# Performance work log

Hardware: AMD Instinct MI355X
Metric: run time of the kernel (lower is better)

Reference implementation:

```python
import jax, jax.numpy as jnp
import numpy as np

B, NMASK, DIM, HEADS = 8, 1024, 768, 12
HEAD_DIM = DIM // HEADS
SCALE = HEAD_DIM ** -0.5
NEG = -1e9  # finite stand-in for -inf to keep fully-masked rows NaN-free


def setup_inputs() -> dict:
    key = jax.random.key(0)
    ks = jax.random.split(key, 7)
    x = jax.random.normal(ks[0], (B, NMASK + 1, DIM), dtype=jnp.float32)
    # valid-prefix padding mask (realistic variable-length batch), lengths >= 1
    lengths = jax.random.randint(ks[1], (B,), 1, NMASK + 1)
    mask = jnp.arange(NMASK)[None, :] < lengths[:, None]  # (B, NMASK) bool
    w_qkv = jax.random.normal(ks[2], (DIM, 3 * DIM), dtype=jnp.float32) * (DIM ** -0.5)
    b_qkv = jax.random.normal(ks[3], (3 * DIM,), dtype=jnp.float32) * 0.02
    w_proj = jax.random.normal(ks[4], (DIM, DIM), dtype=jnp.float32) * (DIM ** -0.5)
    b_proj = jax.random.normal(ks[5], (DIM,), dtype=jnp.float32) * 0.02
    return {"x": x, "mask": mask, "w_qkv": w_qkv, "b_qkv": b_qkv,
            "w_proj": w_proj, "b_proj": b_proj}


def reference(x, mask, w_qkv, b_qkv, w_proj, b_proj):
    b, n, _ = x.shape
    qkv = x @ w_qkv + b_qkv                        # (b, n, 3*dim)
    qkv = qkv.reshape(b, n, 3, HEADS, HEAD_DIM)    # 'b n (qkv h d)'
    qkv = jnp.transpose(qkv, (2, 0, 3, 1, 4))      # (3, b, h, n, d)
    q, k, v = qkv[0], qkv[1], qkv[2]
    logits = jnp.einsum('bhid,bhjd->bhij', q, k) * SCALE
    m = jnp.pad(mask, ((0, 0), (1, 0)), constant_values=True)   # prepend CLS=True
    am = m[:, None, :] & m[:, :, None]             # (b, n, n)
    logits = jnp.where(am[:, None, :, :], logits, NEG)
    attn = jax.nn.softmax(logits, axis=-1)
    out = jnp.einsum('bhij,bhjd->bhid', attn, v)   # (b, h, n, d)
    out = jnp.transpose(out, (0, 2, 1, 3)).reshape(b, n, DIM)
    return out @ w_proj + b_proj                   # dropout is identity (eval/p=0)
```

## Files before the change

### kernel.cpp

```cpp
#include <hip/hip_runtime.h>
#include <stdint.h>

#define BATCH   8
#define NMASK_  1024
#define SEQ     1025
#define NPAD    1056
#define DIM     768
#define HEADS   12
#define HD      64
#define BHN     (BATCH*HEADS)
#define MROWS   (BATCH*SEQ)
#define K3      (3*DIM)

typedef unsigned short u16;
typedef __attribute__((ext_vector_type(8))) short s8v;
typedef __attribute__((ext_vector_type(4))) float f4v;
typedef __attribute__((ext_vector_type(4))) unsigned short u16x4;

__device__ __forceinline__ u16 rne_bf16(float f) {
  unsigned u = __float_as_uint(f);
  u += 0x7fffu + ((u >> 16) & 1u);
  return (u16)(u >> 16);
}
__device__ __forceinline__ float bf2f(u16 u) {
  return __uint_as_float(((unsigned)u) << 16);
}

__device__ __forceinline__ void gld16(const u16* g, u16* l) {
  __builtin_amdgcn_global_load_lds(
      (const __attribute__((address_space(1))) void*)g,
      (__attribute__((address_space(3))) void*)l, 16, 0, 0);
}

__global__ __launch_bounds__(256) void k_len(const int* __restrict__ mask,
                                             int* __restrict__ lens) {
  int b = blockIdx.x, t = threadIdx.x;
  int s = 0;
  for (int j = t; j < NMASK_; j += 256) s += (mask[b * NMASK_ + j] != 0) ? 1 : 0;
  __shared__ int red[256];
  red[t] = s; __syncthreads();
  for (int st = 128; st > 0; st >>= 1) { if (t < st) red[t] += red[t + st]; __syncthreads(); }
  if (t == 0) lens[b] = red[0] + 1;
}

__global__ __launch_bounds__(256) void k_cvt_x(const float* __restrict__ x,
                                               u16* __restrict__ xb, int n4) {
  int i = blockIdx.x * 256 + threadIdx.x;
  if (i >= n4) return;
  float4 v = ((const float4*)x)[i];
  u16x4 o;
  o[0] = rne_bf16(v.x); o[1] = rne_bf16(v.y); o[2] = rne_bf16(v.z); o[3] = rne_bf16(v.w);
  *(u16x4*)&xb[i * 4] = o;
}

__global__ __launch_bounds__(256) void k_wT(const float* __restrict__ w,
                                            u16* __restrict__ wT, int R, int C) {
  __shared__ float tile[32][33];
  int c0 = blockIdx.x * 32, r0 = blockIdx.y * 32;
  int tx = threadIdx.x & 31, ty = threadIdx.x >> 5;
  #pragma unroll
  for (int i = 0; i < 32; i += 8) tile[ty + i][tx] = w[(size_t)(r0 + ty + i) * C + c0 + tx];
  __syncthreads();
  #pragma unroll
  for (int i = 0; i < 32; i += 8)
    wT[(size_t)(c0 + ty + i) * R + r0 + tx] = rne_bf16(tile[tx][ty + i]);
}

__global__ __launch_bounds__(256) void k_zpad(u16* __restrict__ VT) {
  int idx = blockIdx.x * 256 + threadIdx.x;
  const int PADW = NPAD - SEQ;
  if (idx >= BHN * HD * PADW) return;
  int c = idx % PADW, rd = idx / PADW;
  VT[(size_t)rd * NPAD + SEQ + c] = 0;
}

__device__ __forceinline__ void gemm_ml128(const u16* __restrict__ A,
                                           const u16* __restrict__ Bt,
                                           int M, int m0, int n0,
                                           f4v acc[4][4], u16* smem) {
  u16* lA = smem;
  u16* lB = smem + 4096;
  const int t = threadIdx.x;
  const int w = t >> 6, l = t & 63, lg = l >> 4, lr = l & 15;
  const int wr = w >> 1, wc = w & 1;

  int rA0 = m0 + (t >> 2);       if (rA0 >= M) rA0 = M - 1;
  int rA1 = m0 + (t >> 2) + 64;  if (rA1 >= M) rA1 = M - 1;
  const u16* sA0 = A  + (size_t)rA0 * DIM + (t & 3) * 8;
  const u16* sA1 = A  + (size_t)rA1 * DIM + (t & 3) * 8;
  const u16* sB0 = Bt + (size_t)(n0 + (t >> 2)) * DIM + (t & 3) * 8;
  const u16* sB1 = Bt + (size_t)(n0 + (t >> 2) + 64) * DIM + (t & 3) * 8;
  u16* dA0 = &lA[w * 512];
  u16* dA1 = &lA[2048 + w * 512];
  u16* dB0 = &lB[w * 512];
  u16* dB1 = &lB[2048 + w * 512];

  #pragma unroll
  for (int fm = 0; fm < 4; fm++)
    #pragma unroll
    for (int fn = 0; fn < 4; fn++) { f4v z = {0.f, 0.f, 0.f, 0.f}; acc[fm][fn] = z; }

  for (int k0 = 0; k0 < DIM; k0 += 32) {
    __syncthreads();
    gld16(sA0, dA0); gld16(sA1, dA1);
    gld16(sB0, dB0); gld16(sB1, dB1);
    sA0 += 32; sA1 += 32; sB0 += 32; sB1 += 32;
    __syncthreads();
    s8v a[4], bb[4];
    #pragma unroll
    for (int fm = 0; fm < 4; fm++) a[fm] = *(const s8v*)&lA[(wr * 64 + fm * 16 + lr) * 32 + lg * 8];
    #pragma unroll
    for (int fn = 0; fn < 4; fn++) bb[fn] = *(const s8v*)&lB[(wc * 64 + fn * 16 + lr) * 32 + lg * 8];
    #pragma unroll
    for (int fm = 0; fm < 4; fm++)
      #pragma unroll
      for (int fn = 0; fn < 4; fn++)
        acc[fm][fn] = __builtin_amdgcn_mfma_f32_16x16x32_bf16(a[fm], bb[fn], acc[fm][fn], 0, 0, 0);
  }
}

__global__ __launch_bounds__(256) void k_gemm_qkv(const u16* __restrict__ xb,
                                                  const u16* __restrict__ wqkvT,
                                                  const float* __restrict__ bqkv,
                                                  const int* __restrict__ lens,
                                                  u16* __restrict__ Q,
                                                  u16* __restrict__ Kb,
                                                  u16* __restrict__ VT) {
  __shared__ alignas(16) u16 smem[16384];
  int m0 = blockIdx.x * 128, n0 = blockIdx.y * 128;
  const int which = n0 / DIM;
  if (which < 2) {
    int b0 = m0 / SEQ, off = m0 - b0 * SEQ;
    bool spans = (m0 + 127) >= (b0 + 1) * SEQ;
    if (!spans && off >= lens[b0]) return;
  }
  f4v acc[4][4];
  gemm_ml128(xb, wqkvT, MROWS, m0, n0, acc, smem);
  const int t = threadIdx.x;
  const int w = t >> 6, l = t & 63, lg = l >> 4, lr = l & 15;
  const int wr = w >> 1, wc = w & 1;
  const int hbase = (n0 - which * DIM) >> 6;
  const float qs = (which == 0) ? 0.125f : 1.0f;

  __syncthreads();
  #pragma unroll
  for (int fn = 0; fn < 4; fn++) {
    int col = wc * 64 + fn * 16 + lr;
    float bias = bqkv[n0 + col];
    #pragma unroll
    for (int fm = 0; fm < 4; fm++)
      #pragma unroll
      for (int r = 0; r < 4; r++) {
        int row = wr * 64 + fm * 16 + lg * 4 + r;
        smem[row * 128 + col] = rne_bf16((acc[fm][fn][r] + bias) * qs);
      }
  }
  __syncthreads();

  if (which < 2) {
    u16* dst = (which == 0) ? Q : Kb;
    #pragma unroll
    for (int p = 0; p < 8; p++) {
      int c = p * 256 + t;
      int row = c >> 4, col = (c & 15) * 8;
      int gm = m0 + row;
      if (gm >= MROWS) continue;
      int b = gm / SEQ, n = gm - b * SEQ;
      int head = hbase + (col >> 6), d = col & 63;
      *(s8v*)&dst[((size_t)(b * HEADS + head) * NPAD + n) * HD + d] =
          *(const s8v*)&smem[row * 128 + col];
    }
  } else {
    #pragma unroll
    for (int p = 0; p < 8; p++) {
      int c = p * 256 + t;
      int d = c & 127, nb = c >> 7;
      int gm0 = m0 + nb * 8;
      if (gm0 >= MROWS) continue;
      int head = hbase + (d >> 6), dl = d & 63;
      int b0 = gm0 / SEQ;
      if (gm0 + 7 < MROWS && (gm0 + 7) < (b0 + 1) * SEQ) {
        s8v v;
        #pragma unroll
        for (int e = 0; e < 8; e++) v[e] = (short)smem[(nb * 8 + e) * 128 + d];
        int n = gm0 - b0 * SEQ;
        *(s8v*)&VT[((size_t)(b0 * HEADS + head) * HD + dl) * NPAD + n] = v;
      } else {
        for (int e = 0; e < 8; e++) {
          int gm = gm0 + e;
          if (gm >= MROWS) break;
          int b = gm / SEQ, n = gm - b * SEQ;
          VT[((size_t)(b * HEADS + head) * HD + dl) * NPAD + n] = smem[(nb * 8 + e) * 128 + d];
        }
      }
    }
  }
}

__global__ __launch_bounds__(256) void k_vmean(const u16* __restrict__ VT,
                                               float* __restrict__ vmean) {
  int bh = blockIdx.x, t = threadIdx.x;
  int d = t >> 2, part = t & 3;
  const u16* row = VT + (size_t)(bh * HD + d) * NPAD;
  float s = 0.f;
  for (int jc = part * 264; jc < part * 264 + 264; jc += 8) {
    if (jc + 8 <= SEQ) {
      s8v v = *(const s8v*)&row[jc];
      #pragma unroll
      for (int e = 0; e < 8; e++) s += bf2f((u16)v[e]);
    } else {
      for (int e = 0; e < 8; e++) if (jc + e < SEQ) s += bf2f(row[jc + e]);
    }
  }
  __shared__ float red[256];
  red[t] = s; __syncthreads();
  if (part == 0)
    vmean[bh * HD + d] = (red[t] + red[t + 1] + red[t + 2] + red[t + 3]) * (1.0f / (float)SEQ);
}

__global__ __launch_bounds__(256) void k_vproj(const float* __restrict__ vmean,
                                               const u16* __restrict__ wprojT,
                                               const float* __restrict__ bproj,
                                               float* __restrict__ vproj) {
  int gid = blockIdx.x * 4 + (threadIdx.x >> 6);
  if (gid >= BATCH * DIM) return;
  int b = gid / DIM, n = gid - b * DIM;
  int l = threadIdx.x & 63;
  const u16* wr = wprojT + (size_t)n * DIM;
  const float* vm = vmean + b * DIM;
  float s = 0.f;
  #pragma unroll
  for (int i = 0; i < DIM / 64; ++i)
    s += vm[l + i * 64] * bf2f(wr[l + i * 64]);
  #pragma unroll
  for (int off = 32; off >= 1; off >>= 1) s += __shfl_xor(s, off);
  if (l == 0) vproj[gid] = s + bproj[n];
}

__global__ __launch_bounds__(256) void k_attn(const u16* __restrict__ Q,
                                              const u16* __restrict__ Kb,
                                              const u16* __restrict__ VT,
                                              const int* __restrict__ lens,
                                              u16* __restrict__ aout) {
  int bh = blockIdx.x; int b = bh / HEADS, h = bh - b * HEADS;
  int Lp1 = lens[b];
  int q0 = blockIdx.y * 64;
  if (q0 >= Lp1) return;
  __shared__ alignas(16) u16 Kt[64 * 64];
  __shared__ alignas(16) u16 Vt[64 * 64];
  __shared__ alignas(16) u16 Pt[4][16 * 72];
  const int t = threadIdx.x, w = t >> 6, l = t & 63, lg = l >> 4, lr = l & 15;
  const u16* Qbh = Q  + (size_t)bh * NPAD * HD;
  const u16* Kbh = Kb + (size_t)bh * NPAD * HD;
  const u16* Vbh = VT + (size_t)bh * HD * NPAD;

  int qi = q0 + w * 16 + lr;
  s8v qf[2];
  qf[0] = *(const s8v*)&Qbh[(size_t)qi * HD +      lg * 8];
  qf[1] = *(const s8v*)&Qbh[(size_t)qi * HD + 32 + lg * 8];

  f4v o[4];
  #pragma unroll
  for (int fd = 0; fd < 4; fd++) { f4v z = {0.f, 0.f, 0.f, 0.f}; o[fd] = z; }
  float mrow[4], ssacc[4];
  #pragma unroll
  for (int r = 0; r < 4; r++) { mrow[r] = -1e30f; ssacc[r] = 0.f; }

  const int js = t >> 2, cs = t & 3;
  const u16* kSrc = Kbh + (size_t)js * HD   + cs * 8;
  const u16* vSrc = Vbh + (size_t)js * NPAD + cs * 8;
  const int kDst0 = js * 64 + ((cs       ^ (js & 7)) * 8);
  const int kDst1 = js * 64 + (((cs + 4) ^ (js & 7)) * 8);
  s8v kr0, kr1, vr0, vr1;
  kr0 = *(const s8v*)(kSrc);        kr1 = *(const s8v*)(kSrc + 32);
  vr0 = *(const s8v*)(vSrc);        vr1 = *(const s8v*)(vSrc + 32);

  for (int j0 = 0; j0 < Lp1; j0 += 64) {
    __syncthreads();
    *(s8v*)&Kt[kDst0] = kr0;  *(s8v*)&Kt[kDst1] = kr1;
    *(s8v*)&Vt[kDst0] = vr0;  *(s8v*)&Vt[kDst1] = vr1;
    if (j0 + 64 < Lp1) {
      kr0 = *(const s8v*)(kSrc + (size_t)(j0 + 64) * HD);
      kr1 = *(const s8v*)(kSrc + (size_t)(j0 + 64) * HD + 32);
      vr0 = *(const s8v*)(vSrc + (j0 + 64));
      vr1 = *(const s8v*)(vSrc + (j0 + 64) + 32);
    }
    __syncthreads();

    f4v sf[4];
    #pragma unroll
    for (int jf = 0; jf < 4; jf++) { f4v z = {0.f,0.f,0.f,0.f}; sf[jf] = z; }
    __builtin_amdgcn_s_setprio(1);
    #pragma unroll
    for (int jf = 0; jf < 4; jf++) {
      int j = jf * 16 + lr;
      #pragma unroll
      for (int kf = 0; kf < 2; kf++) {
        s8v kfr = *(const s8v*)&Kt[j * 64 + (((kf * 4 + lg) ^ (j & 7)) * 8)];
        sf[jf] = __builtin_amdgcn_mfma_f32_16x16x32_bf16(qf[kf], kfr, sf[jf], 0, 0, 0);
      }
    }
    __builtin_amdgcn_s_setprio(0);

    float sv[4][4], pmax[4];
    if (j0 + 64 <= Lp1) {
      #pragma unroll
      for (int r = 0; r < 4; r++) {
        sv[r][0] = sf[0][r]; sv[r][1] = sf[1][r];
        sv[r][2] = sf[2][r]; sv[r][3] = sf[3][r];
        float tm = fmaxf(fmaxf(sv[r][0], sv[r][1]), fmaxf(sv[r][2], sv[r][3]));
        tm = fmaxf(tm, __shfl_xor(tm, 1)); tm = fmaxf(tm, __shfl_xor(tm, 2));
        tm = fmaxf(tm, __shfl_xor(tm, 4)); tm = fmaxf(tm, __shfl_xor(tm, 8));
        pmax[r] = tm;
      }
    } else {
      bool ok[4];
      #pragma unroll
      for (int jf = 0; jf < 4; jf++) ok[jf] = (j0 + jf * 16 + lr) < Lp1;
      #pragma unroll
      for (int r = 0; r < 4; r++) {
        sv[r][0] = ok[0] ? sf[0][r] : -1e30f;
        sv[r][1] = ok[1] ? sf[1][r] : -1e30f;
        sv[r][2] = ok[2] ? sf[2][r] : -1e30f;
        sv[r][3] = ok[3] ? sf[3][r] : -1e30f;
        float tm = fmaxf(fmaxf(sv[r][0], sv[r][1]), fmaxf(sv[r][2], sv[r][3]));
        tm = fmaxf(tm, __shfl_xor(tm, 1)); tm = fmaxf(tm, __shfl_xor(tm, 2));
        tm = fmaxf(tm, __shfl_xor(tm, 4)); tm = fmaxf(tm, __shfl_xor(tm, 8));
        pmax[r] = tm;
      }
    }
    bool ng = (pmax[0] <= mrow[0] + 8.f) && (pmax[1] <= mrow[1] + 8.f) &&
              (pmax[2] <= mrow[2] + 8.f) && (pmax[3] <= mrow[3] + 8.f);
    if (!__all(ng)) {
      #pragma unroll
      for (int r = 0; r < 4; r++) {
        float nm = fmaxf(mrow[r], pmax[r]);
        float fs = __expf(mrow[r] - nm);
        mrow[r] = nm;
        ssacc[r] *= fs;
        o[0][r] *= fs; o[1][r] *= fs; o[2][r] *= fs; o[3][r] *= fs;
      }
    }
    u16* P = &Pt[w][0];
    #pragma unroll
    for (int r = 0; r < 4; r++) {
      float e0 = __expf(sv[r][0] - mrow[r]);
      float e1 = __expf(sv[r][1] - mrow[r]);
      float e2 = __expf(sv[r][2] - mrow[r]);
      float e3 = __expf(sv[r][3] - mrow[r]);
      int prow = (lg * 4 + r) * 72;
      P[prow +      lr] = rne_bf16(e0);
      P[prow + 16 + lr] = rne_bf16(e1);
      P[prow + 32 + lr] = rne_bf16(e2);
      P[prow + 48 + lr] = rne_bf16(e3);
      ssacc[r] += (e0 + e1) + (e2 + e3);
    }
    asm volatile("s_waitcnt lgkmcnt(0)" ::: "memory");
    s8v pa[2];
    pa[0] = *(const s8v*)&P[lr * 72 +      lg * 8];
    pa[1] = *(const s8v*)&P[lr * 72 + 32 + lg * 8];
    __builtin_amdgcn_s_setprio(1);
    #pragma unroll
    for (int fd = 0; fd < 4; fd++) {
      int dv = fd * 16 + lr;
      #pragma unroll
      for (int kf = 0; kf < 2; kf++) {
        s8v vb = *(const s8v*)&Vt[dv * 64 + (((kf * 4 + lg) ^ (dv & 7)) * 8)];
        o[fd] = __builtin_amdgcn_mfma_f32_16x16x32_bf16(pa[kf], vb, o[fd], 0, 0, 0);
      }
    }
    __builtin_amdgcn_s_setprio(0);
  }

  float inv[4];
  #pragma unroll
  for (int r = 0; r < 4; r++) {
    float rs = ssacc[r];
    rs += __shfl_xor(rs, 1); rs += __shfl_xor(rs, 2);
    rs += __shfl_xor(rs, 4); rs += __shfl_xor(rs, 8);
    inv[r] = 1.0f / rs;
  }
  #pragma unroll
  for (int fd = 0; fd < 4; fd++)
    #pragma unroll
    for (int r = 0; r < 4; r++) {
      int i = q0 + w * 16 + lg * 4 + r;
      if (i < Lp1)
        aout[(size_t)(b * SEQ + i) * DIM + h * HD + fd * 16 + lr] = rne_bf16(o[fd][r] * inv[r]);
    }
}

__global__ __launch_bounds__(256) void k_bcast(const int* __restrict__ lens,
                                               const float* __restrict__ vproj,
                                               float* __restrict__ out) {
  int idx = blockIdx.x * 256 + threadIdx.x;
  if (idx >= MROWS * DIM / 4) return;
  int e4 = idx * 4;
  int b = e4 / (SEQ * DIM);
  int rem = e4 - b * (SEQ * DIM);
  int i = rem / DIM;
  if (i >= lens[b]) {
    int c = rem - i * DIM;
    const float* vp = &vproj[b * DIM + c];
    float4 v = { vp[0], vp[1], vp[2], vp[3] };
    ((float4*)out)[idx] = v;
  }
}

__global__ __launch_bounds__(256) void k_gemm_proj(const u16* __restrict__ aout,
                                                   const u16* __restrict__ wprojT,
                                                   const float* __restrict__ bproj,
                                                   const int* __restrict__ lens,
                                                   float* __restrict__ out) {
  __shared__ alignas(16) u16 smem[16384];
  int m0 = blockIdx.x * 128, n0 = blockIdx.y * 128;
  {
    int b0 = m0 / SEQ, off = m0 - b0 * SEQ;
    bool spans = (m0 + 127) >= (b0 + 1) * SEQ;
    if (!spans && off >= lens[b0]) return;
  }
  f4v acc[4][4];
  gemm_ml128(aout, wprojT, MROWS, m0, n0, acc, smem);
  const int t = threadIdx.x;
  const int w = t >> 6, l = t & 63, lg = l >> 4, lr = l & 15;
  const int wr = w >> 1, wc = w & 1;
  #pragma unroll
  for (int fn = 0; fn < 4; fn++) {
    int gc = n0 + wc * 64 + fn * 16 + lr;
    float bias = bproj[gc];
    #pragma unroll
    for (int fm = 0; fm < 4; fm++)
      #pragma unroll
      for (int r = 0; r < 4; r++) {
        int gm = m0 + wr * 64 + fm * 16 + lg * 4 + r;
        if (gm < MROWS) out[(size_t)gm * DIM + gc] = acc[fm][fn][r] + bias;
      }
  }
}

extern "C" void kernel_launch(void* const* d_in, const int* in_sizes, int n_in,
                              void* d_out, int out_size, void* d_ws, size_t ws_size,
                              hipStream_t stream) {
  const float* x      = (const float*)d_in[0];
  const int*   mask   = (const int*)  d_in[1];
  const float* w_qkv  = (const float*)d_in[2];
  const float* b_qkv  = (const float*)d_in[3];
  const float* w_proj = (const float*)d_in[4];
  const float* b_proj = (const float*)d_in[5];
  float* out = (float*)d_out;

  u16* xb     = (u16*)d_ws;
  u16* wqkvT  = xb    + (size_t)MROWS * DIM;
  u16* wprojT = wqkvT + (size_t)K3 * DIM;
  u16* Q      = wprojT + (size_t)DIM * DIM;
  u16* Kb     = Q     + (size_t)BHN * NPAD * HD;
  u16* VT     = Kb    + (size_t)BHN * NPAD * HD;
  float* vmean = (float*)(VT + (size_t)BHN * NPAD * HD);
  int* lens    = (int*)(vmean + BHN * HD);
  float* vproj = (float*)(lens + 256);
  u16* aout   = xb;

  k_len  <<<dim3(BATCH), dim3(256), 0, stream>>>(mask, lens);
  k_cvt_x<<<dim3((MROWS * DIM / 4 + 255) / 256), dim3(256), 0, stream>>>(x, xb, MROWS * DIM / 4);
  k_wT   <<<dim3(K3 / 32, DIM / 32), dim3(256), 0, stream>>>(w_qkv, wqkvT, DIM, K3);
  k_wT   <<<dim3(DIM / 32, DIM / 32), dim3(256), 0, stream>>>(w_proj, wprojT, DIM, DIM);
  k_zpad <<<dim3((BHN * HD * (NPAD - SEQ) + 255) / 256), dim3(256), 0, stream>>>(VT);
  k_gemm_qkv<<<dim3((MROWS + 127) / 128, K3 / 128), dim3(256), 0, stream>>>(xb, wqkvT, b_qkv, lens, Q, Kb, VT);
  k_vmean<<<dim3(BHN), dim3(256), 0, stream>>>(VT, vmean);
  k_vproj<<<dim3((BATCH * DIM + 3) / 4), dim3(256), 0, stream>>>(vmean, wprojT, b_proj, vproj);
  k_attn <<<dim3(BHN, (SEQ + 63) / 64), dim3(256), 0, stream>>>(Q, Kb, VT, lens, aout);
  k_gemm_proj<<<dim3((MROWS + 127) / 128, DIM / 128), dim3(256), 0, stream>>>(aout, wprojT, b_proj, lens, out);
  k_bcast<<<dim3((MROWS * DIM / 4 + 255) / 256), dim3(256), 0, stream>>>(lens, vproj, out);
}
```

Measured before the change: 179.3 us.

## Process two KV tiles per iteration and reverse query-block launch order

Result: slower. 185.7 us (+3.6%).

```diff
diff --git a/kernel.cpp b/kernel.cpp
--- a/kernel.cpp
+++ b/kernel.cpp
@@ -244,11 +244,11 @@
                                               u16* __restrict__ aout) {
   int bh = blockIdx.x; int b = bh / HEADS, h = bh - b * HEADS;
   int Lp1 = lens[b];
-  int q0 = blockIdx.y * 64;
+  int q0 = ((int)gridDim.y - 1 - (int)blockIdx.y) * 64;
   if (q0 >= Lp1) return;
-  __shared__ alignas(16) u16 Kt[64 * 64];
-  __shared__ alignas(16) u16 Vt[64 * 64];
-  __shared__ alignas(16) u16 Pt[4][16 * 72];
+  __shared__ alignas(16) u16 Kt[2][64 * 64];
+  __shared__ alignas(16) u16 Vt[2][64 * 64];
+  __shared__ alignas(16) u16 Pt[4][2][16 * 72];
   const int t = threadIdx.x, w = t >> 6, l = t & 63, lg = l >> 4, lr = l & 15;
   const u16* Qbh = Q  + (size_t)bh * NPAD * HD;
   const u16* Kbh = Kb + (size_t)bh * NPAD * HD;
@@ -271,63 +271,86 @@
   const u16* vSrc = Vbh + (size_t)js * NPAD + cs * 8;
   const int kDst0 = js * 64 + ((cs       ^ (js & 7)) * 8);
   const int kDst1 = js * 64 + (((cs + 4) ^ (js & 7)) * 8);
-  s8v kr0, kr1, vr0, vr1;
-  kr0 = *(const s8v*)(kSrc);        kr1 = *(const s8v*)(kSrc + 32);
-  vr0 = *(const s8v*)(vSrc);        vr1 = *(const s8v*)(vSrc + 32);
-
-  for (int j0 = 0; j0 < Lp1; j0 += 64) {
+  s8v krA0, krA1, vrA0, vrA1, krB0, krB1, vrB0, vrB1;
+  krA0 = *(const s8v*)(kSrc);        krA1 = *(const s8v*)(kSrc + 32);
+  vrA0 = *(const s8v*)(vSrc);        vrA1 = *(const s8v*)(vSrc + 32);
+  if (64 < Lp1) {
+    krB0 = *(const s8v*)(kSrc + (size_t)64 * HD);
+    krB1 = *(const s8v*)(kSrc + (size_t)64 * HD + 32);
+    vrB0 = *(const s8v*)(vSrc + 64);
+    vrB1 = *(const s8v*)(vSrc + 64 + 32);
+  }
+
+  for (int j0 = 0; j0 < Lp1; j0 += 128) {
+    const bool hasB  = (j0 + 64)  < Lp1;
+    const bool fullA = (j0 + 64)  <= Lp1;
+    const bool fullB = (j0 + 128) <= Lp1;
     __syncthreads();
-    *(s8v*)&Kt[kDst0] = kr0;  *(s8v*)&Kt[kDst1] = kr1;
-    *(s8v*)&Vt[kDst0] = vr0;  *(s8v*)&Vt[kDst1] = vr1;
-    if (j0 + 64 < Lp1) {
-      kr0 = *(const s8v*)(kSrc + (size_t)(j0 + 64) * HD);
-      kr1 = *(const s8v*)(kSrc + (size_t)(j0 + 64) * HD + 32);
-      vr0 = *(const s8v*)(vSrc + (j0 + 64));
-      vr1 = *(const s8v*)(vSrc + (j0 + 64) + 32);
+    *(s8v*)&Kt[0][kDst0] = krA0;  *(s8v*)&Kt[0][kDst1] = krA1;
+    *(s8v*)&Vt[0][kDst0] = vrA0;  *(s8v*)&Vt[0][kDst1] = vrA1;
+    if (hasB) {
+      *(s8v*)&Kt[1][kDst0] = krB0;  *(s8v*)&Kt[1][kDst1] = krB1;
+      *(s8v*)&Vt[1][kDst0] = vrB0;  *(s8v*)&Vt[1][kDst1] = vrB1;
+    }
+    if (j0 + 128 < Lp1) {
+      krA0 = *(const s8v*)(kSrc + (size_t)(j0 + 128) * HD);
+      krA1 = *(const s8v*)(kSrc + (size_t)(j0 + 128) * HD + 32);
+      vrA0 = *(const s8v*)(vSrc + (j0 + 128));
+      vrA1 = *(const s8v*)(vSrc + (j0 + 128) + 32);
+    }
+    if (j0 + 192 < Lp1) {
+      krB0 = *(const s8v*)(kSrc + (size_t)(j0 + 192) * HD);
+      krB1 = *(const s8v*)(kSrc + (size_t)(j0 + 192) * HD + 32);
+      vrB0 = *(const s8v*)(vSrc + (j0 + 192));
+      vrB1 = *(const s8v*)(vSrc + (j0 + 192) + 32);
     }
     __syncthreads();
 
-    f4v sf[4];
-    #pragma unroll
-    for (int jf = 0; jf < 4; jf++) { f4v z = {0.f,0.f,0.f,0.f}; sf[jf] = z; }
+    f4v sfA[4], sfB[4];
+    #pragma unroll
+    for (int jf = 0; jf < 4; jf++) { f4v z = {0.f,0.f,0.f,0.f}; sfA[jf] = z; sfB[jf] = z; }
     __builtin_amdgcn_s_setprio(1);
     #pragma unroll
     for (int jf = 0; jf < 4; jf++) {
       int j = jf * 16 + lr;
       #pragma unroll
       for (int kf = 0; kf < 2; kf++) {
-        s8v kfr = *(const s8v*)&Kt[j * 64 + (((kf * 4 + lg) ^ (j & 7)) * 8)];
-        sf[jf] = __builtin_amdgcn_mfma_f32_16x16x32_bf16(qf[kf], kfr, sf[jf], 0, 0, 0);
+        s8v kfr = *(const s8v*)&Kt[0][j * 64 + (((kf * 4 + lg) ^ (j & 7)) * 8)];
+        sfA[jf] = __builtin_amdgcn_mfma_f32_16x16x32_bf16(qf[kf], kfr, sfA[jf], 0, 0, 0);
+      }
+    }
+    if (hasB) {
+      #pragma unroll
+      for (int jf = 0; jf < 4; jf++) {
+        int j = jf * 16 + lr;
+        #pragma unroll
+        for (int kf = 0; kf < 2; kf++) {
+          s8v kfr = *(const s8v*)&Kt[1][j * 64 + (((kf * 4 + lg) ^ (j & 7)) * 8)];
+          sfB[jf] = __builtin_amdgcn_mfma_f32_16x16x32_bf16(qf[kf], kfr, sfB[jf], 0, 0, 0);
+        }
       }
     }
     __builtin_amdgcn_s_setprio(0);
 
-    float sv[4][4], pmax[4];
-    if (j0 + 64 <= Lp1) {
-      #pragma unroll
-      for (int r = 0; r < 4; r++) {
-        sv[r][0] = sf[0][r]; sv[r][1] = sf[1][r];
-        sv[r][2] = sf[2][r]; sv[r][3] = sf[3][r];
-        float tm = fmaxf(fmaxf(sv[r][0], sv[r][1]), fmaxf(sv[r][2], sv[r][3]));
-        tm = fmaxf(tm, __shfl_xor(tm, 1)); tm = fmaxf(tm, __shfl_xor(tm, 2));
-        tm = fmaxf(tm, __shfl_xor(tm, 4)); tm = fmaxf(tm, __shfl_xor(tm, 8));
-        pmax[r] = tm;
-      }
-    } else {
-      bool ok[4];
-      #pragma unroll
-      for (int jf = 0; jf < 4; jf++) ok[jf] = (j0 + jf * 16 + lr) < Lp1;
-      #pragma unroll
-      for (int r = 0; r < 4; r++) {
-        sv[r][0] = ok[0] ? sf[0][r] : -1e30f;
-        sv[r][1] = ok[1] ? sf[1][r] : -1e30f;
-        sv[r][2] = ok[2] ? sf[2][r] : -1e30f;
-        sv[r][3] = ok[3] ? sf[3][r] : -1e30f;
-        float tm = fmaxf(fmaxf(sv[r][0], sv[r][1]), fmaxf(sv[r][2], sv[r][3]));
-        tm = fmaxf(tm, __shfl_xor(tm, 1)); tm = fmaxf(tm, __shfl_xor(tm, 2));
-        tm = fmaxf(tm, __shfl_xor(tm, 4)); tm = fmaxf(tm, __shfl_xor(tm, 8));
-        pmax[r] = tm;
-      }
+    float svA[4][4], svB[4][4], pmax[4];
+    bool okA[4], okB[4];
+    #pragma unroll
+    for (int jf = 0; jf < 4; jf++) {
+      okA[jf] = fullA || ((j0 + jf * 16 + lr) < Lp1);
+      okB[jf] = hasB && (fullB || ((j0 + 64 + jf * 16 + lr) < Lp1));
+    }
+    #pragma unroll
+    for (int r = 0; r < 4; r++) {
+      #pragma unroll
+      for (int jf = 0; jf < 4; jf++) {
+        svA[r][jf] = okA[jf] ? sfA[jf][r] : -1e30f;
+        svB[r][jf] = okB[jf] ? sfB[jf][r] : -1e30f;
+      }
+      float tm = fmaxf(fmaxf(fmaxf(svA[r][0], svA[r][1]), fmaxf(svA[r][2], svA[r][3])),
+                       fmaxf(fmaxf(svB[r][0], svB[r][1]), fmaxf(svB[r][2], svB[r][3])));
+      tm = fmaxf(tm, __shfl_xor(tm, 1)); tm = fmaxf(tm, __shfl_xor(tm, 2));
+      tm = fmaxf(tm, __shfl_xor(tm, 4)); tm = fmaxf(tm, __shfl_xor(tm, 8));
+      pmax[r] = tm;
     }
     bool ng = (pmax[0] <= mrow[0] + 8.f) && (pmax[1] <= mrow[1] + 8.f) &&
               (pmax[2] <= mrow[2] + 8.f) && (pmax[3] <= mrow[3] + 8.f);
@@ -341,32 +364,60 @@
         o[0][r] *= fs; o[1][r] *= fs; o[2][r] *= fs; o[3][r] *= fs;
       }
     }
-    u16* P = &Pt[w][0];
+    u16* PA = &Pt[w][0][0];
+    u16* PB = &Pt[w][1][0];
     #pragma unroll
     for (int r = 0; r < 4; r++) {
-      float e0 = __expf(sv[r][0] - mrow[r]);
-      float e1 = __expf(sv[r][1] - mrow[r]);
-      float e2 = __expf(sv[r][2] - mrow[r]);
-      float e3 = __expf(sv[r][3] - mrow[r]);
       int prow = (lg * 4 + r) * 72;
-      P[prow +      lr] = rne_bf16(e0);
-      P[prow + 16 + lr] = rne_bf16(e1);
-      P[prow + 32 + lr] = rne_bf16(e2);
-      P[prow + 48 + lr] = rne_bf16(e3);
-      ssacc[r] += (e0 + e1) + (e2 + e3);
+      float eA0 = __expf(svA[r][0] - mrow[r]);
+      float eA1 = __expf(svA[r][1] - mrow[r]);
+      float eA2 = __expf(svA[r][2] - mrow[r]);
+      float eA3 = __expf(svA[r][3] - mrow[r]);
+      PA[prow +      lr] = rne_bf16(eA0);
+      PA[prow + 16 + lr] = rne_bf16(eA1);
+      PA[prow + 32 + lr] = rne_bf16(eA2);
+      PA[prow + 48 + lr] = rne_bf16(eA3);
+      float sum = (eA0 + eA1) + (eA2 + eA3);
+      if (hasB) {
+        float eB0 = __expf(svB[r][0] - mrow[r]);
+        float eB1 = __expf(svB[r][1] - mrow[r]);
+        float eB2 = __expf(svB[r][2] - mrow[r]);
+        float eB3 = __expf(svB[r][3] - mrow[r]);
+        PB[prow +      lr] = rne_bf16(eB0);
+        PB[prow + 16 + lr] = rne_bf16(eB1);
+        PB[prow + 32 + lr] = rne_bf16(eB2);
+        PB[prow + 48 + lr] = rne_bf16(eB3);
+        sum += (eB0 + eB1) + (eB2 + eB3);
+      }
+      ssacc[r] += sum;
     }
     asm volatile("s_waitcnt lgkmcnt(0)" ::: "memory");
-    s8v pa[2];
-    pa[0] = *(const s8v*)&P[lr * 72 +      lg * 8];
-    pa[1] = *(const s8v*)&P[lr * 72 + 32 + lg * 8];
+    s8v paA[2], paB[2];
+    paA[0] = *(const s8v*)&PA[lr * 72 +      lg * 8];
+    paA[1] = *(const s8v*)&PA[lr * 72 + 32 + lg * 8];
+    if (hasB) {
+      paB[0] = *(const s8v*)&PB[lr * 72 +      lg * 8];
+      paB[1] = *(const s8v*)&PB[lr * 72 + 32 + lg * 8];
+    }
     __builtin_amdgcn_s_setprio(1);
     #pragma unroll
     for (int fd = 0; fd < 4; fd++) {
       int dv = fd * 16 + lr;
       #pragma unroll
       for (int kf = 0; kf < 2; kf++) {
-        s8v vb = *(const s8v*)&Vt[dv * 64 + (((kf * 4 + lg) ^ (dv & 7)) * 8)];
-        o[fd] = __builtin_amdgcn_mfma_f32_16x16x32_bf16(pa[kf], vb, o[fd], 0, 0, 0);
+        s8v vb = *(const s8v*)&Vt[0][dv * 64 + (((kf * 4 + lg) ^ (dv & 7)) * 8)];
+        o[fd] = __builtin_amdgcn_mfma_f32_16x16x32_bf16(paA[kf], vb, o[fd], 0, 0, 0);
+      }
+    }
+    if (hasB) {
+      #pragma unroll
+      for (int fd = 0; fd < 4; fd++) {
+        int dv = fd * 16 + lr;
+        #pragma unroll
+        for (int kf = 0; kf < 2; kf++) {
+          s8v vb = *(const s8v*)&Vt[1][dv * 64 + (((kf * 4 + lg) ^ (dv & 7)) * 8)];
+          o[fd] = __builtin_amdgcn_mfma_f32_16x16x32_bf16(paB[kf], vb, o[fd], 0, 0, 0);
+        }
       }
     }
     __builtin_amdgcn_s_setprio(0);
```
